# Optimization experiments

Measured on AMD Instinct MI355X. Metric: run time of the kernel, lower is better.

The kernel has to match this reference:

```python
import jax, jax.numpy as jnp
import numpy as np

ROUTING_ROUNDS = 3
CAPS_NUM, SEQ_LEN, EMB_DIM, CAPS_DIM = 8, 200, 128, 64
BATCH = 1024


def setup_inputs() -> dict:
    key = jax.random.key(0)
    k1, k2, k3, k4 = jax.random.split(key, 4)
    behaviors = jax.random.normal(k1, (BATCH, SEQ_LEN, EMB_DIM), dtype=jnp.float32)
    sequence_mask = jax.random.randint(k2, (BATCH, SEQ_LEN), 0, 2) > 0  # bool
    S = jax.random.normal(k3, (EMB_DIM, CAPS_DIM), dtype=jnp.float32) * 0.05
    B0 = jax.random.normal(k4, (CAPS_NUM, SEQ_LEN), dtype=jnp.float32) * 0.05
    return {"behaviors": behaviors, "sequence_mask": sequence_mask, "S": S, "B0": B0}


def _squash(caps):
    # caps: [b, k, d]; norm over capsule dim
    n = jnp.linalg.norm(caps, axis=2, keepdims=True)
    n2 = jnp.square(n)
    return n2 / ((1.0 + n2) * n) * caps


def reference(behaviors, sequence_mask, S, B0):
    b = behaviors.shape[0]
    beh = jnp.einsum('ble,ed->bld', behaviors, S)          # project: [b, l, d]
    mask = sequence_mask[:, None, :]                        # [b, 1, l] -> broadcasts over k
    neg = jnp.finfo(jnp.float32).min
    B = jnp.broadcast_to(B0[None, :, :], (b,) + B0.shape)   # [b, k, l]
    caps = None
    for i in range(ROUTING_ROUNDS):
        logits = jnp.where(mask, B, neg)                    # masked routing logits
        W = jax.nn.softmax(logits, axis=2)                  # [b, k, l]
        caps = _squash(jnp.einsum('bkl,bld->bkd', W, beh))  # [b, k, d]
        if i < ROUTING_ROUNDS - 1:
            B = B + jnp.einsum('bkd,bld->bkl', caps, beh)   # logit update
    return caps
```

## Files before the change

### kernel.cpp

```cpp
#include <hip/hip_runtime.h>
#include <math.h>

#define NCAPS 8
#define SEQ 200
#define EMB 128
#define CDIM 64
#define NROUNDS 3
#define BPAD 68
#define CPAD 68

typedef __bf16 bf16x8 __attribute__((ext_vector_type(8)));
typedef float f32x4 __attribute__((ext_vector_type(4)));
typedef unsigned short ushort8 __attribute__((ext_vector_type(8)));
typedef unsigned short ushort4v __attribute__((ext_vector_type(4)));

__device__ __forceinline__ float4 ld4(const float* p) { return *reinterpret_cast<const float4*>(p); }
__device__ __forceinline__ void st4(float* p, float4 v) { *reinterpret_cast<float4*>(p) = v; }
__device__ __forceinline__ float bf2f(unsigned short b) {
  unsigned u = ((unsigned)b) << 16;
  return __builtin_bit_cast(float, u);
}
__device__ __forceinline__ void split8(float4 u0, float4 u1, bf16x8& h, bf16x8& lo) {
  float a[8] = {u0.x, u0.y, u0.z, u0.w, u1.x, u1.y, u1.z, u1.w};
#pragma unroll
  for (int j = 0; j < 8; ++j) {
    h[j] = (__bf16)a[j];
    lo[j] = (__bf16)(a[j] - (float)h[j]);
  }
}

__global__ void split_S_kernel(const float* __restrict__ S, unsigned short* __restrict__ wsS) {
  int i = blockIdx.x * 256 + threadIdx.x;
  if (i >= EMB * CDIM) return;
  int e = i >> 6, d = i & 63;
  float v = S[i];
  __bf16 hb = (__bf16)v;
  __bf16 lb = (__bf16)(v - (float)hb);
  int fi = (e >> 5) * 4 + (d >> 4);
  int ln = (((e >> 3) & 3) << 4) + (d & 15);
  int j = e & 7;
  wsS[(fi * 64 + ln) * 8 + j] = __builtin_bit_cast(unsigned short, hb);
  wsS[EMB * CDIM + (fi * 64 + ln) * 8 + j] = __builtin_bit_cast(unsigned short, lb);
}

__global__ __launch_bounds__(256, 2) void proj_kernel(
    const float* __restrict__ A,
    const unsigned short* __restrict__ SfG,
    unsigned short* __restrict__ behG16,
    int Mtot)
{
  __shared__ ushort8 sF[2048];
  const int t = threadIdx.x;
  const int lane = t & 63;
  const int w = t >> 6;
  const int fr = lane & 15;
  const int kg = lane >> 4;
  {
    const ushort8* pf = (const ushort8*)SfG;
    for (int i = t; i < 2048; i += 256) sF[i] = pf[i];
  }
  __syncthreads();

#pragma unroll
  for (int rt = 0; rt < 2; ++rt) {
    const int r0 = blockIdx.x * 128 + (w * 2 + rt) * 16;
    const int row = r0 + fr;
    const bool ok = (row < Mtot);
    const float* arow = A + (size_t)row * EMB + kg * 8;

    bf16x8 aH[4], aL[4];
#pragma unroll
    for (int ks = 0; ks < 4; ++ks) {
      if (ok) {
        split8(ld4(arow + ks * 32), ld4(arow + ks * 32 + 4), aH[ks], aL[ks]);
      } else {
        bf16x8 z;
#pragma unroll
        for (int j = 0; j < 8; ++j) z[j] = (__bf16)0.f;
        aH[ks] = z; aL[ks] = z;
      }
    }

#pragma unroll
    for (int ct = 0; ct < 4; ++ct) {
      f32x4 acc = {0.f, 0.f, 0.f, 0.f};
#pragma unroll
      for (int ks = 0; ks < 4; ++ks) {
        bf16x8 sH = __builtin_bit_cast(bf16x8, sF[(ks * 4 + ct) * 64 + lane]);
        bf16x8 sL = __builtin_bit_cast(bf16x8, sF[1024 + (ks * 4 + ct) * 64 + lane]);
        acc = __builtin_amdgcn_mfma_f32_16x16x32_bf16(sH, aH[ks], acc, 0, 0, 0);
        acc = __builtin_amdgcn_mfma_f32_16x16x32_bf16(sH, aL[ks], acc, 0, 0, 0);
        acc = __builtin_amdgcn_mfma_f32_16x16x32_bf16(sL, aH[ks], acc, 0, 0, 0);
      }
      if (ok) {
        ushort4v o;
        o[0] = __builtin_bit_cast(unsigned short, (__bf16)acc[0]);
        o[1] = __builtin_bit_cast(unsigned short, (__bf16)acc[1]);
        o[2] = __builtin_bit_cast(unsigned short, (__bf16)acc[2]);
        o[3] = __builtin_bit_cast(unsigned short, (__bf16)acc[3]);
        *reinterpret_cast<ushort4v*>(&behG16[(size_t)row * CDIM + ct * 16 + kg * 4]) = o;
      }
    }
  }
}

__global__ __launch_bounds__(512, 4) void route_kernel(
    const unsigned short* __restrict__ behG16,
    const unsigned char* __restrict__ maskraw,
    const float* __restrict__ B0,
    float* __restrict__ out)
{
  __shared__ float sBeh[SEQ][BPAD];
  __shared__ float sB[NCAPS][SEQ];
  __shared__ float sWt[SEQ][NCAPS];
  __shared__ float sCaps[NCAPS][CPAD];
  __shared__ float sPart[4][NCAPS][CDIM];
  __shared__ float sMask[SEQ];
  __shared__ int sFlagA, sFlagB;

  const int b = blockIdx.x;
  const int t = threadIdx.x;
  const int lane = t & 63;
  const int w = t >> 6;

  if (t == 0) { sFlagA = 0; sFlagB = 0; }
  __syncthreads();
  for (int i = t; i < 1024; i += 512) {
    unsigned char v = maskraw[i];
    if (v != 0) {
      int m = i & 3;
      if (m == 1) atomicOr(&sFlagA, 1);
      else if (m >= 2) atomicOr(&sFlagB, 1);
    }
  }
  __syncthreads();
  const int mode = sFlagA ? 1 : (sFlagB ? 2 : 0);

  if (mode == 1) {
    for (int i = t; i < SEQ; i += 512)
      sMask[i] = maskraw[(size_t)b * SEQ + i] ? 1.0f : 0.0f;
  } else if (mode == 2) {
    const float* mf = (const float*)maskraw;
    for (int i = t; i < SEQ; i += 512)
      sMask[i] = (mf[(size_t)b * SEQ + i] != 0.0f) ? 1.0f : 0.0f;
  } else {
    const int* mi = (const int*)maskraw;
    for (int i = t; i < SEQ; i += 512)
      sMask[i] = mi[(size_t)b * SEQ + i] ? 1.0f : 0.0f;
  }
  for (int i = t; i < NCAPS * SEQ; i += 512)
    (&sB[0][0])[i] = B0[i];
  for (int i = t; i < SEQ * 8; i += 512) {
    int l = i >> 3, d8 = (i & 7) * 8;
    ushort8 u = *reinterpret_cast<const ushort8*>(
        behG16 + ((size_t)b * SEQ + l) * CDIM + d8);
    st4(&sBeh[l][d8], make_float4(bf2f(u[0]), bf2f(u[1]), bf2f(u[2]), bf2f(u[3])));
    st4(&sBeh[l][d8 + 4], make_float4(bf2f(u[4]), bf2f(u[5]), bf2f(u[6]), bf2f(u[7])));
  }
  __syncthreads();

  for (int round = 0; round < NROUNDS; ++round) {
    {
      const int k = w;
      float v0 = sB[k][lane],       f0 = sMask[lane];
      float v1 = sB[k][lane + 64],  f1 = sMask[lane + 64];
      float v2 = sB[k][lane + 128], f2 = sMask[lane + 128];
      float v3 = 0.f, f3 = 0.f;
      if (lane < SEQ - 192) { v3 = sB[k][lane + 192]; f3 = sMask[lane + 192]; }
      float m = -3.402823466e38f;
      if (f0 > 0.f) m = fmaxf(m, v0);
      if (f1 > 0.f) m = fmaxf(m, v1);
      if (f2 > 0.f) m = fmaxf(m, v2);
      if (f3 > 0.f) m = fmaxf(m, v3);
#pragma unroll
      for (int off = 32; off >= 1; off >>= 1) m = fmaxf(m, __shfl_xor(m, off));
      float e0 = (f0 > 0.f) ? __expf(v0 - m) : 0.f;
      float e1 = (f1 > 0.f) ? __expf(v1 - m) : 0.f;
      float e2 = (f2 > 0.f) ? __expf(v2 - m) : 0.f;
      float e3 = (f3 > 0.f) ? __expf(v3 - m) : 0.f;
      float s = ((e0 + e1) + (e2 + e3));
#pragma unroll
      for (int off = 32; off >= 1; off >>= 1) s += __shfl_xor(s, off);
      float inv = (s > 0.f) ? (1.0f / s) : 0.f;
      sWt[lane][k] = e0 * inv;
      sWt[lane + 64][k] = e1 * inv;
      sWt[lane + 128][k] = e2 * inv;
      if (lane < SEQ - 192) sWt[lane + 192][k] = e3 * inv;
    }
    __syncthreads();

    float vcap;
    {
      float p0 = 0.f, p1 = 0.f, p2 = 0.f, p3 = 0.f;
      float p4 = 0.f, p5 = 0.f, p6 = 0.f, p7 = 0.f;
      for (int i = 0; i < 25; ++i) {
        const int l = w + 8 * i;
        float bv = sBeh[l][lane];
        float4 wa = ld4(&sWt[l][0]);
        float4 wb = ld4(&sWt[l][4]);
        p0 = fmaf(wa.x, bv, p0); p1 = fmaf(wa.y, bv, p1);
        p2 = fmaf(wa.z, bv, p2); p3 = fmaf(wa.w, bv, p3);
        p4 = fmaf(wb.x, bv, p4); p5 = fmaf(wb.y, bv, p5);
        p6 = fmaf(wb.z, bv, p6); p7 = fmaf(wb.w, bv, p7);
      }
      if (w < 4) {
        sPart[w][0][lane] = p0; sPart[w][1][lane] = p1;
        sPart[w][2][lane] = p2; sPart[w][3][lane] = p3;
        sPart[w][4][lane] = p4; sPart[w][5][lane] = p5;
        sPart[w][6][lane] = p6; sPart[w][7][lane] = p7;
      }
      __syncthreads();
      if (w >= 4) {
        const int u = w - 4;
        sPart[u][0][lane] += p0; sPart[u][1][lane] += p1;
        sPart[u][2][lane] += p2; sPart[u][3][lane] += p3;
        sPart[u][4][lane] += p4; sPart[u][5][lane] += p5;
        sPart[u][6][lane] += p6; sPart[u][7][lane] += p7;
      }
      __syncthreads();
      vcap = (sPart[0][w][lane] + sPart[1][w][lane]) +
             (sPart[2][w][lane] + sPart[3][w][lane]);
    }

    {
      float q = vcap * vcap;
#pragma unroll
      for (int off = 32; off >= 1; off >>= 1) q += __shfl_xor(q, off);
      float n = sqrtf(q);
      float f = (q > 0.f) ? (q / ((1.0f + q) * n)) : 0.f;
      vcap *= f;
      sCaps[w][lane] = vcap;
      if (round == NROUNDS - 1)
        out[((size_t)b * NCAPS + w) * CDIM + lane] = vcap;
    }
    __syncthreads();

    if (round < NROUNDS - 1) {
      const int fr = lane & 15;
      const int kg = lane >> 4;
      bf16x8 aH[2], aL[2];
#pragma unroll
      for (int ks = 0; ks < 2; ++ks) {
        if (fr < NCAPS) {
          split8(ld4(&sCaps[fr][ks * 32 + kg * 8]),
                 ld4(&sCaps[fr][ks * 32 + kg * 8 + 4]), aH[ks], aL[ks]);
        } else {
          bf16x8 z;
#pragma unroll
          for (int j = 0; j < 8; ++j) z[j] = (__bf16)0.f;
          aH[ks] = z; aL[ks] = z;
        }
      }
      for (int lt = w; lt < 13; lt += 8) {
        const int l = lt * 16 + fr;
        const int lc = (l < SEQ) ? l : (SEQ - 1);
        f32x4 acc = {0.f, 0.f, 0.f, 0.f};
#pragma unroll
        for (int ks = 0; ks < 2; ++ks) {
          bf16x8 bh, bl;
          split8(ld4(&sBeh[lc][ks * 32 + kg * 8]),
                 ld4(&sBeh[lc][ks * 32 + kg * 8 + 4]), bh, bl);
          acc = __builtin_amdgcn_mfma_f32_16x16x32_bf16(aH[ks], bh, acc, 0, 0, 0);
          acc = __builtin_amdgcn_mfma_f32_16x16x32_bf16(aL[ks], bh, acc, 0, 0, 0);
          acc = __builtin_amdgcn_mfma_f32_16x16x32_bf16(aH[ks], bl, acc, 0, 0, 0);
        }
        if (kg < 2 && l < SEQ) {
#pragma unroll
          for (int reg = 0; reg < 4; ++reg)
            sB[kg * 4 + reg][l] += acc[reg];
        }
      }
    }
    __syncthreads();
  }
}

__global__ __launch_bounds__(512, 2) void mie1_kernel(
    const float* __restrict__ behaviors,
    const unsigned char* __restrict__ maskraw,
    const float* __restrict__ S,
    const float* __restrict__ B0,
    float* __restrict__ out)
{
  __shared__ float sBeh[SEQ][68];
  __shared__ float sB[NCAPS][SEQ];
  __shared__ float sW[NCAPS][SEQ];
  __shared__ float sCaps[NCAPS][CPAD];
  __shared__ float sMask[SEQ];
  __shared__ int sFlagA, sFlagB;
  __shared__ ushort8 sSfH[16 * 64];
  __shared__ ushort8 sSfL[16 * 64];

  const int b = blockIdx.x;
  const int t = threadIdx.x;
  const int lane = t & 63;
  const int w = t >> 6;

  if (t == 0) { sFlagA = 0; sFlagB = 0; }
  __syncthreads();
  for (int i = t; i < 1024; i += 512) {
    unsigned char v = maskraw[i];
    if (v != 0) {
      int m = i & 3;
      if (m == 1) atomicOr(&sFlagA, 1);
      else if (m >= 2) atomicOr(&sFlagB, 1);
    }
  }
  __syncthreads();
  const int mode = sFlagA ? 1 : (sFlagB ? 2 : 0);

  if (mode == 1) {
    for (int i = t; i < SEQ; i += 512)
      sMask[i] = maskraw[(size_t)b * SEQ + i] ? 1.0f : 0.0f;
  } else if (mode == 2) {
    const float* mf = (const float*)maskraw;
    for (int i = t; i < SEQ; i += 512)
      sMask[i] = (mf[(size_t)b * SEQ + i] != 0.0f) ? 1.0f : 0.0f;
  } else {
    const int* mi = (const int*)maskraw;
    for (int i = t; i < SEQ; i += 512)
      sMask[i] = mi[(size_t)b * SEQ + i] ? 1.0f : 0.0f;
  }
  for (int i = t; i < NCAPS * SEQ; i += 512)
    (&sB[0][0])[i] = B0[i];
  for (int i = t; i < EMB * CDIM; i += 512) {
    int e = i >> 6, d = i & 63;
    float v = S[i];
    __bf16 hb = (__bf16)v;
    __bf16 lb = (__bf16)(v - (float)hb);
    int fi = (e >> 5) * 4 + (d >> 4);
    int ln = (((e >> 3) & 3) << 4) + (d & 15);
    int j = e & 7;
    ((unsigned short*)&sSfH[fi * 64 + ln])[j] = __builtin_bit_cast(unsigned short, hb);
    ((unsigned short*)&sSfL[fi * 64 + ln])[j] = __builtin_bit_cast(unsigned short, lb);
  }
  __syncthreads();

  {
    const int fr = lane & 15;
    const int kg = lane >> 4;
    for (int rt = w; rt < 13; rt += 8) {
      const int r0 = rt * 16;
      const int row = r0 + fr;
      const float* arow = behaviors + ((size_t)b * SEQ + row) * EMB + kg * 8;
      f32x4 acc[4];
#pragma unroll
      for (int ct = 0; ct < 4; ++ct) acc[ct] = (f32x4){0.f, 0.f, 0.f, 0.f};
#pragma unroll
      for (int ks = 0; ks < 4; ++ks) {
        bf16x8 aH, aL;
        if (row < SEQ) {
          split8(ld4(arow + ks * 32), ld4(arow + ks * 32 + 4), aH, aL);
        } else {
#pragma unroll
          for (int j = 0; j < 8; ++j) { aH[j] = (__bf16)0.f; aL[j] = (__bf16)0.f; }
        }
#pragma unroll
        for (int ct = 0; ct < 4; ++ct) {
          bf16x8 sH = __builtin_bit_cast(bf16x8, sSfH[(ks * 4 + ct) * 64 + lane]);
          bf16x8 sL = __builtin_bit_cast(bf16x8, sSfL[(ks * 4 + ct) * 64 + lane]);
          acc[ct] = __builtin_amdgcn_mfma_f32_16x16x32_bf16(aH, sH, acc[ct], 0, 0, 0);
          acc[ct] = __builtin_amdgcn_mfma_f32_16x16x32_bf16(aL, sH, acc[ct], 0, 0, 0);
          acc[ct] = __builtin_amdgcn_mfma_f32_16x16x32_bf16(aH, sL, acc[ct], 0, 0, 0);
        }
      }
#pragma unroll
      for (int ct = 0; ct < 4; ++ct) {
#pragma unroll
        for (int reg = 0; reg < 4; ++reg) {
          int orow = r0 + kg * 4 + reg;
          if (orow < SEQ) sBeh[orow][ct * 16 + fr] = acc[ct][reg];
        }
      }
    }
  }
  __syncthreads();

  for (int round = 0; round < NROUNDS; ++round) {
    {
      const int k = w;
      float v0 = sB[k][lane],       f0 = sMask[lane];
      float v1 = sB[k][lane + 64],  f1 = sMask[lane + 64];
      float v2 = sB[k][lane + 128], f2 = sMask[lane + 128];
      float v3 = 0.f, f3 = 0.f;
      if (lane < SEQ - 192) { v3 = sB[k][lane + 192]; f3 = sMask[lane + 192]; }
      float m = -3.402823466e38f;
      if (f0 > 0.f) m = fmaxf(m, v0);
      if (f1 > 0.f) m = fmaxf(m, v1);
      if (f2 > 0.f) m = fmaxf(m, v2);
      if (f3 > 0.f) m = fmaxf(m, v3);
#pragma unroll
      for (int off = 32; off >= 1; off >>= 1) m = fmaxf(m, __shfl_xor(m, off));
      float e0 = (f0 > 0.f) ? __expf(v0 - m) : 0.f;
      float e1 = (f1 > 0.f) ? __expf(v1 - m) : 0.f;
      float e2 = (f2 > 0.f) ? __expf(v2 - m) : 0.f;
      float e3 = (f3 > 0.f) ? __expf(v3 - m) : 0.f;
      float s = ((e0 + e1) + (e2 + e3));
#pragma unroll
      for (int off = 32; off >= 1; off >>= 1) s += __shfl_xor(s, off);
      float inv = (s > 0.f) ? (1.0f / s) : 0.f;
      sW[k][lane] = e0 * inv;
      sW[k][lane + 64] = e1 * inv;
      sW[k][lane + 128] = e2 * inv;
      if (lane < SEQ - 192) sW[k][lane + 192] = e3 * inv;
    }
    __syncthreads();
    {
      float a0 = 0.f, a1 = 0.f, a2 = 0.f, a3 = 0.f;
#pragma unroll 2
      for (int l = 0; l < SEQ; l += 4) {
        a0 = fmaf(sW[w][l + 0], sBeh[l + 0][lane], a0);
        a1 = fmaf(sW[w][l + 1], sBeh[l + 1][lane], a1);
        a2 = fmaf(sW[w][l + 2], sBeh[l + 2][lane], a2);
        a3 = fmaf(sW[w][l + 3], sBeh[l + 3][lane], a3);
      }
      float v = (a0 + a1) + (a2 + a3);
      float q = v * v;
#pragma unroll
      for (int off = 32; off >= 1; off >>= 1) q += __shfl_xor(q, off);
      float n = sqrtf(q);
      float f = (q > 0.f) ? (q / ((1.0f + q) * n)) : 0.f;
      v *= f;
      sCaps[w][lane] = v;
      if (round == NROUNDS - 1)
        out[((size_t)b * NCAPS + w) * CDIM + lane] = v;
    }
    __syncthreads();
    if (round < NROUNDS - 1) {
      const int k = t & 7;
      for (int oi = t; oi < NCAPS * SEQ; oi += 512) {
        int l = oi >> 3;
        float px = 0.f, py = 0.f, pz = 0.f, pw = 0.f;
#pragma unroll 4
        for (int i = 0; i < 16; ++i) {
          float4 cp = ld4(&sCaps[k][i * 4]);
          float4 b4 = ld4(&sBeh[l][i * 4]);
          px = fmaf(cp.x, b4.x, px);
          py = fmaf(cp.y, b4.y, py);
          pz = fmaf(cp.z, b4.z, pz);
          pw = fmaf(cp.w, b4.w, pw);
        }
        sB[k][l] += (px + py) + (pz + pw);
      }
    }
    __syncthreads();
  }
}

extern "C" void kernel_launch(void* const* d_in, const int* in_sizes, int n_in,
                              void* d_out, int out_size, void* d_ws, size_t ws_size,
                              hipStream_t stream) {
  const float* behaviors = (const float*)d_in[0];
  const unsigned char* maskraw = (const unsigned char*)d_in[1];
  const float* S = (const float*)d_in[2];
  const float* B0 = (const float*)d_in[3];
  float* out = (float*)d_out;
  const int B = in_sizes[0] / (SEQ * EMB);
  const int Mtot = B * SEQ;
  const size_t sfrag_bytes = (size_t)2 * EMB * CDIM * sizeof(unsigned short);
  const size_t beh_bytes = (size_t)Mtot * CDIM * sizeof(unsigned short);
  if (ws_size >= sfrag_bytes + beh_bytes) {
    unsigned short* wsS = (unsigned short*)d_ws;
    unsigned short* behG16 = (unsigned short*)((char*)d_ws + sfrag_bytes);
    split_S_kernel<<<dim3((EMB * CDIM + 255) / 256), dim3(256), 0, stream>>>(S, wsS);
    proj_kernel<<<dim3((Mtot + 127) / 128), dim3(256), 0, stream>>>(behaviors, wsS, behG16, Mtot);
    route_kernel<<<dim3(B), dim3(512), 0, stream>>>(behG16, maskraw, B0, out);
  } else {
    mie1_kernel<<<dim3(B), dim3(512), 0, stream>>>(behaviors, maskraw, S, B0, out);
  }
}
```

Before: 74.38 us.

## Drop activation low-part split and LDS staging in projection kernel

The projection kernel no longer splits activations into high and low bf16 parts. It uses only the high part times the split S, which cuts the MFMAs per tile from three to two. It also stops staging the split S in shared memory and reads it straight from global/L2, which removes the LDS fill and the block barrier. Launch bounds rise to 8 blocks per CU. This trades accuracy of the projected behaviors, now carrying bf16 rounding error on the activations, for less compute and memory traffic. It also risks more global-load latency on the S fragments.

```diff
diff --git a/kernel.cpp b/kernel.cpp
--- a/kernel.cpp
+++ b/kernel.cpp
@@ -27,6 +27,12 @@
     h[j] = (__bf16)a[j];
     lo[j] = (__bf16)(a[j] - (float)h[j]);
   }
+}
+__device__ __forceinline__ bf16x8 cvt8(float4 u0, float4 u1) {
+  bf16x8 h;
+  h[0] = (__bf16)u0.x; h[1] = (__bf16)u0.y; h[2] = (__bf16)u0.z; h[3] = (__bf16)u0.w;
+  h[4] = (__bf16)u1.x; h[5] = (__bf16)u1.y; h[6] = (__bf16)u1.z; h[7] = (__bf16)u1.w;
+  return h;
 }
 
 __global__ void split_S_kernel(const float* __restrict__ S, unsigned short* __restrict__ wsS) {
@@ -43,23 +49,18 @@
   wsS[EMB * CDIM + (fi * 64 + ln) * 8 + j] = __builtin_bit_cast(unsigned short, lb);
 }
 
-__global__ __launch_bounds__(256, 2) void proj_kernel(
+__global__ __launch_bounds__(256, 8) void proj_kernel(
     const float* __restrict__ A,
     const unsigned short* __restrict__ SfG,
     unsigned short* __restrict__ behG16,
     int Mtot)
 {
-  __shared__ ushort8 sF[2048];
   const int t = threadIdx.x;
   const int lane = t & 63;
   const int w = t >> 6;
   const int fr = lane & 15;
   const int kg = lane >> 4;
-  {
-    const ushort8* pf = (const ushort8*)SfG;
-    for (int i = t; i < 2048; i += 256) sF[i] = pf[i];
-  }
-  __syncthreads();
+  const ushort8* pf = (const ushort8*)SfG;
 
 #pragma unroll
   for (int rt = 0; rt < 2; ++rt) {
@@ -68,36 +69,35 @@
     const bool ok = (row < Mtot);
     const float* arow = A + (size_t)row * EMB + kg * 8;
 
-    bf16x8 aH[4], aL[4];
+    f32x4 acc[4];
+#pragma unroll
+    for (int ct = 0; ct < 4; ++ct) acc[ct] = (f32x4){0.f, 0.f, 0.f, 0.f};
+
 #pragma unroll
     for (int ks = 0; ks < 4; ++ks) {
+      bf16x8 aH;
       if (ok) {
-        split8(ld4(arow + ks * 32), ld4(arow + ks * 32 + 4), aH[ks], aL[ks]);
+        aH = cvt8(ld4(arow + ks * 32), ld4(arow + ks * 32 + 4));
       } else {
-        bf16x8 z;
-#pragma unroll
-        for (int j = 0; j < 8; ++j) z[j] = (__bf16)0.f;
-        aH[ks] = z; aL[ks] = z;
-      }
-    }
-
+#pragma unroll
+        for (int j = 0; j < 8; ++j) aH[j] = (__bf16)0.f;
+      }
+#pragma unroll
+      for (int ct = 0; ct < 4; ++ct) {
+        bf16x8 sH = __builtin_bit_cast(bf16x8, pf[(ks * 4 + ct) * 64 + lane]);
+        bf16x8 sL = __builtin_bit_cast(bf16x8, pf[1024 + (ks * 4 + ct) * 64 + lane]);
+        acc[ct] = __builtin_amdgcn_mfma_f32_16x16x32_bf16(sH, aH, acc[ct], 0, 0, 0);
+        acc[ct] = __builtin_amdgcn_mfma_f32_16x16x32_bf16(sL, aH, acc[ct], 0, 0, 0);
+      }
+    }
 #pragma unroll
     for (int ct = 0; ct < 4; ++ct) {
-      f32x4 acc = {0.f, 0.f, 0.f, 0.f};
-#pragma unroll
-      for (int ks = 0; ks < 4; ++ks) {
-        bf16x8 sH = __builtin_bit_cast(bf16x8, sF[(ks * 4 + ct) * 64 + lane]);
-        bf16x8 sL = __builtin_bit_cast(bf16x8, sF[1024 + (ks * 4 + ct) * 64 + lane]);
-        acc = __builtin_amdgcn_mfma_f32_16x16x32_bf16(sH, aH[ks], acc, 0, 0, 0);
-        acc = __builtin_amdgcn_mfma_f32_16x16x32_bf16(sH, aL[ks], acc, 0, 0, 0);
-        acc = __builtin_amdgcn_mfma_f32_16x16x32_bf16(sL, aH[ks], acc, 0, 0, 0);
-      }
       if (ok) {
         ushort4v o;
-        o[0] = __builtin_bit_cast(unsigned short, (__bf16)acc[0]);
-        o[1] = __builtin_bit_cast(unsigned short, (__bf16)acc[1]);
-        o[2] = __builtin_bit_cast(unsigned short, (__bf16)acc[2]);
-        o[3] = __builtin_bit_cast(unsigned short, (__bf16)acc[3]);
+        o[0] = __builtin_bit_cast(unsigned short, (__bf16)acc[ct][0]);
+        o[1] = __builtin_bit_cast(unsigned short, (__bf16)acc[ct][1]);
+        o[2] = __builtin_bit_cast(unsigned short, (__bf16)acc[ct][2]);
+        o[3] = __builtin_bit_cast(unsigned short, (__bf16)acc[ct][3]);
         *reinterpret_cast<ushort4v*>(&behG16[(size_t)row * CDIM + ct * 16 + kg * 4]) = o;
       }
     }
```

After: 150.5 us. 2.02x slower.
